# Kernel optimization log

Hardware: AMD Instinct MI355X
Metric: run time of the kernel (lower is better)

Reference implementation:

```python
import jax, jax.numpy as jnp
import numpy as np

NUM_BLOCKS = 16
IN_FEATURES = 4096
OUT_FEATURES = 4096
BLOCK_IN = IN_FEATURES // NUM_BLOCKS
BLOCK_OUT = OUT_FEATURES // NUM_BLOCKS
BATCH = 16384


def setup_inputs() -> dict:
    key = jax.random.key(0)
    kx, kw, kb = jax.random.split(key, 3)
    x = jax.random.normal(kx, (BATCH, IN_FEATURES), dtype=jnp.float32)
    # Per-block weights, matching torch nn.Linear init scale (U[-1/sqrt(in), 1/sqrt(in)])
    bound = 1.0 / np.sqrt(BLOCK_IN)
    W = jax.random.uniform(kw, (NUM_BLOCKS, BLOCK_OUT, BLOCK_IN), minval=-bound, maxval=bound, dtype=jnp.float32)
    b = jax.random.uniform(kb, (NUM_BLOCKS, BLOCK_OUT), minval=-bound, maxval=bound, dtype=jnp.float32)
    return {"x": x, "W": W, "b": b}


def reference(x, W, b):
    # x: [N, in_features] -> [N, nb, block_in]
    n = x.shape[0]
    xb = x.reshape(n, NUM_BLOCKS, BLOCK_IN)
    # per-block linear: y = x @ W_k.T + b_k  (fused block-diagonal GEMM)
    yb = jnp.einsum('nki,koi->nko', xb, W) + b  # [N, nb, block_out]
    return yb.reshape(n, OUT_FEATURES)
```

## Files before the change

### kernel.cpp

```cpp
#include <hip/hip_runtime.h>

typedef short short8 __attribute__((ext_vector_type(8)));
typedef float floatx4 __attribute__((ext_vector_type(4)));

#define INF 4096

__device__ __forceinline__ ushort f2bf(float f) {
  unsigned u = __builtin_bit_cast(unsigned, f);
  u += 0x7fffu + ((u >> 16) & 1u);
  return (ushort)(u >> 16);
}

__global__ __launch_bounds__(256, 2) void bd_gemm(
    const float* __restrict__ x, const float* __restrict__ W,
    const float* __restrict__ bias, float* __restrict__ out)
{
  __shared__ ushort lds[2 * 20480];

  const int bid = blockIdx.x;
  const int swz = (bid & 7) * 512 + (bid >> 3);
  const int kblk = swz >> 8;
  const int mt   = swz & 255;
  const int tid  = threadIdx.x;
  const int lane = tid & 63;
  const int wc   = tid >> 6;

  const float* xb = x + (size_t)mt * 64 * INF + kblk * 256;
  const float* wb = W + (size_t)kblk * 256 * 256;

  floatx4 fa[2][2];
  floatx4 fb[8][2];
  floatx4 acc[4][4];
#pragma unroll
  for (int i = 0; i < 4; ++i)
#pragma unroll
    for (int j = 0; j < 4; ++j)
#pragma unroll
      for (int e = 0; e < 4; ++e) acc[i][j][e] = 0.0f;

#define LOADA(kk)                                                    \
  _Pragma("unroll") for (int p = 0; p < 2; ++p) {                    \
    const int id = tid + p * 256;                                    \
    const int r = id >> 3, cc = id & 7;                              \
    const float* s = xb + (size_t)r * INF + (kk) * 64 + cc * 8;      \
    fa[p][0] = *(const floatx4*)s;                                   \
    fa[p][1] = *(const floatx4*)(s + 4);                             \
  }

#define LOADB(kk)                                                    \
  _Pragma("unroll") for (int p = 0; p < 8; ++p) {                    \
    const int id = tid + p * 256;                                    \
    const int r = id >> 3, cc = id & 7;                              \
    const float* s = wb + (size_t)r * 256 + (kk) * 64 + cc * 8;      \
    fb[p][0] = *(const floatx4*)s;                                   \
    fb[p][1] = *(const floatx4*)(s + 4);                             \
  }

#define STORE(buf)                                                           \
  _Pragma("unroll") for (int p = 0; p < 2; ++p) {                            \
    const int id = tid + p * 256;                                            \
    const int r = id >> 3, cc = id & 7;                                      \
    short8 u;                                                                \
    _Pragma("unroll") for (int j = 0; j < 4; ++j) {                          \
      u[j] = (short)f2bf(fa[p][0][j]);                                       \
      u[4 + j] = (short)f2bf(fa[p][1][j]);                                   \
    }                                                                        \
    *(short8*)&lds[(buf) * 20480 + r * 64 + ((cc ^ (r & 7)) << 3)] = u;      \
  }                                                                          \
  _Pragma("unroll") for (int p = 0; p < 8; ++p) {                            \
    const int id = tid + p * 256;                                            \
    const int r = id >> 3, cc = id & 7;                                      \
    short8 u;                                                                \
    _Pragma("unroll") for (int j = 0; j < 4; ++j) {                          \
      u[j] = (short)f2bf(fb[p][0][j]);                                       \
      u[4 + j] = (short)f2bf(fb[p][1][j]);                                   \
    }                                                                        \
    *(short8*)&lds[(buf) * 20480 + 4096 + r * 64 + ((cc ^ (r & 7)) << 3)] = u; \
  }

#define COMPUTE(buf)                                                         \
  _Pragma("unroll") for (int ks = 0; ks < 2; ++ks) {                         \
    const int ko = ks * 32 + ((lane >> 4) << 3);                             \
    const int cc = ko >> 3;                                                  \
    short8 afr[4], bfr[4];                                                   \
    _Pragma("unroll") for (int mi = 0; mi < 4; ++mi) {                       \
      const int r = mi * 16 + (lane & 15);                                   \
      afr[mi] = *(const short8*)&lds[(buf) * 20480 + r * 64 + ((cc ^ (r & 7)) << 3)]; \
    }                                                                        \
    _Pragma("unroll") for (int ni = 0; ni < 4; ++ni) {                       \
      const int r = wc * 64 + ni * 16 + (lane & 15);                         \
      bfr[ni] = *(const short8*)&lds[(buf) * 20480 + 4096 + r * 64 + ((cc ^ (r & 7)) << 3)]; \
    }                                                                        \
    _Pragma("unroll") for (int mi = 0; mi < 4; ++mi)                         \
      _Pragma("unroll") for (int ni = 0; ni < 4; ++ni)                       \
        acc[mi][ni] = __builtin_amdgcn_mfma_f32_16x16x32_bf16(               \
            afr[mi], bfr[ni], acc[mi][ni], 0, 0, 0);                         \
  }

  LOADA(0) LOADB(0) STORE(0)
  __syncthreads();

#pragma unroll
  for (int kk = 0; kk < 4; ++kk) {
    const int cur = kk & 1;
    if (kk < 3) { LOADA(kk + 1) LOADB(kk + 1) }
    COMPUTE(cur)
    if (kk < 3) {
      STORE(cur ^ 1)
      __syncthreads();
    }
  }

  const float* bp = bias + kblk * 256;
  float bv[4];
#pragma unroll
  for (int ni = 0; ni < 4; ++ni) bv[ni] = bp[wc * 64 + ni * 16 + (lane & 15)];

  float* ob = out + (size_t)mt * 64 * INF + kblk * 256;
#pragma unroll
  for (int mi = 0; mi < 4; ++mi) {
#pragma unroll
    for (int ni = 0; ni < 4; ++ni) {
      const int col = wc * 64 + ni * 16 + (lane & 15);
#pragma unroll
      for (int j = 0; j < 4; ++j) {
        const int row = mi * 16 + ((lane >> 4) << 2) + j;
        ob[(size_t)row * INF + col] = acc[mi][ni][j] + bv[ni];
      }
    }
  }

#undef LOADA
#undef LOADB
#undef STORE
#undef COMPUTE
}

extern "C" void kernel_launch(void* const* d_in, const int* in_sizes, int n_in,
                              void* d_out, int out_size, void* d_ws, size_t ws_size,
                              hipStream_t stream) {
  const float* x = (const float*)d_in[0];
  const float* W = (const float*)d_in[1];
  const float* b = (const float*)d_in[2];
  float* out = (float*)d_out;
  hipLaunchKernelGGL(bd_gemm, dim3(4096), dim3(256), 0, stream, x, W, b, out);
}
```

Measured before the change: 131.8 us.

## Make blocks persistent per weight block, keeping W resident in LDS

```diff
diff --git a/kernel.cpp b/kernel.cpp
--- a/kernel.cpp
+++ b/kernel.cpp
@@ -11,129 +11,101 @@
   return (ushort)(u >> 16);
 }
 
-__global__ __launch_bounds__(256, 2) void bd_gemm(
+__global__ __launch_bounds__(512, 2) void bd_gemm(
     const float* __restrict__ x, const float* __restrict__ W,
     const float* __restrict__ bias, float* __restrict__ out)
 {
-  __shared__ ushort lds[2 * 20480];
+  __shared__ ushort wlds[256 * 256];
 
-  const int bid = blockIdx.x;
-  const int swz = (bid & 7) * 512 + (bid >> 3);
-  const int kblk = swz >> 8;
-  const int mt   = swz & 255;
+  const int bid  = blockIdx.x;
+  const int kb   = bid >> 4;
+  const int mg   = bid & 15;
   const int tid  = threadIdx.x;
   const int lane = tid & 63;
-  const int wc   = tid >> 6;
+  const int wid  = tid >> 6;
+  const int wm   = wid >> 1;
+  const int wn   = wid & 1;
+  const int ln   = lane & 15;
+  const int lk   = lane >> 4;
 
-  const float* xb = x + (size_t)mt * 64 * INF + kblk * 256;
-  const float* wb = W + (size_t)kblk * 256 * 256;
+  floatx4 sA[2][4][2];
+  const float* xp = x + ((size_t)mg * 1024 + wm * 16 + ln) * INF + kb * 256 + lk * 8;
 
-  floatx4 fa[2][2];
-  floatx4 fb[8][2];
-  floatx4 acc[4][4];
-#pragma unroll
-  for (int i = 0; i < 4; ++i)
-#pragma unroll
-    for (int j = 0; j < 4; ++j)
-#pragma unroll
-      for (int e = 0; e < 4; ++e) acc[i][j][e] = 0.0f;
-
-#define LOADA(kk)                                                    \
-  _Pragma("unroll") for (int p = 0; p < 2; ++p) {                    \
-    const int id = tid + p * 256;                                    \
-    const int r = id >> 3, cc = id & 7;                              \
-    const float* s = xb + (size_t)r * INF + (kk) * 64 + cc * 8;      \
-    fa[p][0] = *(const floatx4*)s;                                   \
-    fa[p][1] = *(const floatx4*)(s + 4);                             \
+#define LOADH(buf, t, h)                                                    \
+  _Pragma("unroll") for (int q = 0; q < 4; ++q) {                           \
+    const float* s_ = xp + (size_t)(t) * 64 * INF + ((h) * 4 + q) * 32;     \
+    sA[buf][q][0] = *(const floatx4*)s_;                                    \
+    sA[buf][q][1] = *(const floatx4*)(s_ + 4);                              \
   }
 
-#define LOADB(kk)                                                    \
-  _Pragma("unroll") for (int p = 0; p < 8; ++p) {                    \
-    const int id = tid + p * 256;                                    \
-    const int r = id >> 3, cc = id & 7;                              \
-    const float* s = wb + (size_t)r * 256 + (kk) * 64 + cc * 8;      \
-    fb[p][0] = *(const floatx4*)s;                                   \
-    fb[p][1] = *(const floatx4*)(s + 4);                             \
+  LOADH(0, 0, 0)
+
+  {
+    const float* wsrc = W + (size_t)kb * 65536;
+#pragma unroll
+    for (int p = 0; p < 16; ++p) {
+      const int id = tid + p * 512;
+      const int n  = id >> 5;
+      const int kc = id & 31;
+      const float* s_ = wsrc + n * 256 + kc * 8;
+      floatx4 v0 = *(const floatx4*)s_;
+      floatx4 v1 = *(const floatx4*)(s_ + 4);
+      short8 u;
+#pragma unroll
+      for (int j = 0; j < 4; ++j) {
+        u[j]     = (short)f2bf(v0[j]);
+        u[4 + j] = (short)f2bf(v1[j]);
+      }
+      *(short8*)&wlds[n * 256 + ((kc ^ (n & 7)) << 3)] = u;
+    }
+  }
+  __syncthreads();
+
+  float bv[8];
+  {
+    const float* bp = bias + kb * 256 + wn * 128 + ln;
+#pragma unroll
+    for (int ni = 0; ni < 8; ++ni) bv[ni] = bp[ni * 16];
   }
 
-#define STORE(buf)                                                           \
-  _Pragma("unroll") for (int p = 0; p < 2; ++p) {                            \
-    const int id = tid + p * 256;                                            \
-    const int r = id >> 3, cc = id & 7;                                      \
-    short8 u;                                                                \
-    _Pragma("unroll") for (int j = 0; j < 4; ++j) {                          \
-      u[j] = (short)f2bf(fa[p][0][j]);                                       \
-      u[4 + j] = (short)f2bf(fa[p][1][j]);                                   \
-    }                                                                        \
-    *(short8*)&lds[(buf) * 20480 + r * 64 + ((cc ^ (r & 7)) << 3)] = u;      \
-  }                                                                          \
-  _Pragma("unroll") for (int p = 0; p < 8; ++p) {                            \
-    const int id = tid + p * 256;                                            \
-    const int r = id >> 3, cc = id & 7;                                      \
-    short8 u;                                                                \
-    _Pragma("unroll") for (int j = 0; j < 4; ++j) {                          \
-      u[j] = (short)f2bf(fb[p][0][j]);                                       \
-      u[4 + j] = (short)f2bf(fb[p][1][j]);                                   \
-    }                                                                        \
-    *(short8*)&lds[(buf) * 20480 + 4096 + r * 64 + ((cc ^ (r & 7)) << 3)] = u; \
+  floatx4 acc[8];
+  float* op = out + ((size_t)mg * 1024 + wm * 16 + lk * 4) * INF + kb * 256 + wn * 128 + ln;
+
+#define COMPH(buf, h)                                                          \
+  _Pragma("unroll") for (int q = 0; q < 4; ++q) {                              \
+    short8 af;                                                                 \
+    _Pragma("unroll") for (int j = 0; j < 4; ++j) {                            \
+      af[j]     = (short)f2bf(sA[buf][q][0][j]);                               \
+      af[4 + j] = (short)f2bf(sA[buf][q][1][j]);                               \
+    }                                                                          \
+    const int cc = ((h) * 4 + q) * 4 + lk;                                     \
+    _Pragma("unroll") for (int ni = 0; ni < 8; ++ni) {                         \
+      const int n = wn * 128 + ni * 16 + ln;                                   \
+      const short8 bf = *(const short8*)&wlds[n * 256 + ((cc ^ (n & 7)) << 3)];\
+      acc[ni] = __builtin_amdgcn_mfma_f32_16x16x32_bf16(af, bf, acc[ni], 0, 0, 0); \
+    }                                                                          \
   }
 
-#define COMPUTE(buf)                                                         \
-  _Pragma("unroll") for (int ks = 0; ks < 2; ++ks) {                         \
-    const int ko = ks * 32 + ((lane >> 4) << 3);                             \
-    const int cc = ko >> 3;                                                  \
-    short8 afr[4], bfr[4];                                                   \
-    _Pragma("unroll") for (int mi = 0; mi < 4; ++mi) {                       \
-      const int r = mi * 16 + (lane & 15);                                   \
-      afr[mi] = *(const short8*)&lds[(buf) * 20480 + r * 64 + ((cc ^ (r & 7)) << 3)]; \
-    }                                                                        \
-    _Pragma("unroll") for (int ni = 0; ni < 4; ++ni) {                       \
-      const int r = wc * 64 + ni * 16 + (lane & 15);                         \
-      bfr[ni] = *(const short8*)&lds[(buf) * 20480 + 4096 + r * 64 + ((cc ^ (r & 7)) << 3)]; \
-    }                                                                        \
-    _Pragma("unroll") for (int mi = 0; mi < 4; ++mi)                         \
-      _Pragma("unroll") for (int ni = 0; ni < 4; ++ni)                       \
-        acc[mi][ni] = __builtin_amdgcn_mfma_f32_16x16x32_bf16(               \
-            afr[mi], bfr[ni], acc[mi][ni], 0, 0, 0);                         \
+  for (int t = 0; t < 16; ++t) {
+#pragma unroll
+    for (int ni = 0; ni < 8; ++ni)
+#pragma unroll
+      for (int e = 0; e < 4; ++e) acc[ni][e] = 0.0f;
+
+    LOADH(1, t, 1)
+    COMPH(0, 0)
+    if (t < 15) LOADH(0, t + 1, 0)
+    COMPH(1, 1)
+
+#pragma unroll
+    for (int ni = 0; ni < 8; ++ni)
+#pragma unroll
+      for (int j = 0; j < 4; ++j)
+        op[((size_t)t * 64 + j) * INF + ni * 16] = acc[ni][j] + bv[ni];
   }
 
-  LOADA(0) LOADB(0) STORE(0)
-  __syncthreads();
-
-#pragma unroll
-  for (int kk = 0; kk < 4; ++kk) {
-    const int cur = kk & 1;
-    if (kk < 3) { LOADA(kk + 1) LOADB(kk + 1) }
-    COMPUTE(cur)
-    if (kk < 3) {
-      STORE(cur ^ 1)
-      __syncthreads();
-    }
-  }
-
-  const float* bp = bias + kblk * 256;
-  float bv[4];
-#pragma unroll
-  for (int ni = 0; ni < 4; ++ni) bv[ni] = bp[wc * 64 + ni * 16 + (lane & 15)];
-
-  float* ob = out + (size_t)mt * 64 * INF + kblk * 256;
-#pragma unroll
-  for (int mi = 0; mi < 4; ++mi) {
-#pragma unroll
-    for (int ni = 0; ni < 4; ++ni) {
-      const int col = wc * 64 + ni * 16 + (lane & 15);
-#pragma unroll
-      for (int j = 0; j < 4; ++j) {
-        const int row = mi * 16 + ((lane >> 4) << 2) + j;
-        ob[(size_t)row * INF + col] = acc[mi][ni][j] + bv[ni];
-      }
-    }
-  }
-
-#undef LOADA
-#undef LOADB
-#undef STORE
-#undef COMPUTE
+#undef LOADH
+#undef COMPH
 }
 
 extern "C" void kernel_launch(void* const* d_in, const int* in_sizes, int n_in,
@@ -143,5 +115,5 @@
   const float* W = (const float*)d_in[1];
   const float* b = (const float*)d_in[2];
   float* out = (float*)d_out;
-  hipLaunchKernelGGL(bd_gemm, dim3(4096), dim3(256), 0, stream, x, W, b, out);
+  hipLaunchKernelGGL(bd_gemm, dim3(256), dim3(512), 0, stream, x, W, b, out);
 }
```

Result: slower. 246.5 us (+87.1%).
